# Optimization experiments

Hardware: AMD Instinct MI355X
Metric: run time of the kernel (lower is better)

Reference implementation:

```python
import jax, jax.numpy as jnp
import numpy as np
import math

B, L, D = 2, 2048, 768
H, DK = 8, 64
DV = D // H  # 96
N_POS = 32
DFF = 2 * D
EPS = 1e-5


def setup_inputs() -> dict:
    key = jax.random.key(0)
    ks = jax.random.split(key, 12)
    s = 0.02
    return {
        "x": jax.random.normal(ks[0], (B, L, D), jnp.float32),
        "norm1_w": jnp.ones((D,), jnp.float32),
        "norm2_w": jnp.ones((D,), jnp.float32),
        "wq": jax.random.normal(ks[1], (D, H * DK), jnp.float32) * s,
        "wk": jax.random.normal(ks[2], (D, H * DK), jnp.float32) * s,
        "wv": jax.random.normal(ks[3], (D, H * DV), jnp.float32) * s,
        "wo": jax.random.normal(ks[4], (H * DV, D), jnp.float32) * s,
        "bo": jnp.zeros((D,), jnp.float32),
        "u_param": jax.random.normal(ks[5], (H, DK), jnp.float32) * s,
        "v_param": jax.random.normal(ks[6], (H, DK), jnp.float32) * s,
        "w_pos": jax.random.normal(ks[7], (H, DK, N_POS), jnp.float32) * s,
        "w1": jax.random.normal(ks[8], (D, DFF), jnp.float32) * s,
        "b1": jnp.zeros((DFF,), jnp.float32),
        "w2": jax.random.normal(ks[9], (DFF, D), jnp.float32) * s,
        "b2": jnp.zeros((D,), jnp.float32),
    }


def _rel_basis(l: int, n: int) -> jnp.ndarray:
    # Enformer-style central-mask relative position basis: [l, l, n]
    pos = jnp.arange(l)
    distance = pos[None, :] - pos[:, None]  # [l, l]
    pow_rate = jnp.exp(jnp.log(jnp.float32((l + 1) / 2.0)) / (n // 2))
    center_widths = pow_rate ** jnp.arange(1, n // 2 + 1, dtype=jnp.float32)
    d = distance[:, :, None].astype(jnp.float32)
    unsigned = (jnp.abs(d) <= center_widths).astype(jnp.float32)
    signed = jnp.sign(d) * unsigned
    return jnp.concatenate([unsigned, signed], axis=-1)  # [l, l, n]


def _rmsnorm(x, w):
    norm = jnp.mean(x * x, axis=-1, keepdims=True)
    return x * jax.lax.rsqrt(norm + EPS) * w


def reference(x, norm1_w, norm2_w, wq, wk, wv, wo, bo,
              u_param, v_param, w_pos, w1, b1, w2, b2):
    b, l, _ = x.shape
    skip = x
    h1 = _rmsnorm(x, norm1_w)

    q = (h1 @ wq).reshape(b, l, H, DK)
    k = (h1 @ wk).reshape(b, l, H, DK)
    v = (h1 @ wv).reshape(b, l, H, DV)

    basis = _rel_basis(l, N_POS)  # [l, l, n]
    scale = 1.0 / math.sqrt(DK)

    # qr_term: contract q with w_pos first, then with basis (avoids [h,l,l,d] r)
    qw = jnp.einsum('bihd,hdn->bihn', q, w_pos)          # [b,l,h,n]
    qr = jnp.einsum('bihn,ijn->bhij', qw, basis)          # [b,h,l,l]
    uk = jnp.einsum('hd,bjhd->bhj', u_param, k)[:, :, None, :]  # [b,h,1,l]
    vw = jnp.einsum('hd,hdn->hn', v_param, w_pos)         # [h,n]
    vr = jnp.einsum('hn,ijn->hij', vw, basis)[None]       # [1,h,l,l]

    bias = (qr + uk + vr) * scale
    scores = jnp.einsum('bihd,bjhd->bhij', q, k) * scale + bias
    attn = jax.nn.softmax(scores, axis=-1)
    out = jnp.einsum('bhij,bjhd->bihd', attn, v)          # [b,l,h,dv]

    out = out.reshape(b, l, H * DV) @ wo + bo
    x = out + skip

    skip = x
    h2 = _rmsnorm(x, norm2_w)
    h2 = jax.nn.gelu(h2 @ w1 + b1, approximate=False) @ w2 + b2
    return h2 + skip
```

## Files before the change

### kernel.cpp

```cpp
#include <hip/hip_runtime.h>

#define B_ 2
#define L_ 2048
#define D_ 768
#define H_ 8
#define DK_ 64
#define DV_ 96
#define NPOS_ 32

typedef __attribute__((ext_vector_type(8))) __bf16 bf16x8;
typedef __attribute__((ext_vector_type(4))) __bf16 bf16x4;
typedef __attribute__((ext_vector_type(4))) float f32x4;

static __device__ __forceinline__ float bs2f(short s) {
    return (float)__builtin_bit_cast(__bf16, s);
}
static __device__ __forceinline__ short f2bs(float f) {
    return __builtin_bit_cast(short, (__bf16)f);
}

typedef __attribute__((address_space(1))) void gas_void;
typedef __attribute__((address_space(3))) void las_void;
static __device__ __forceinline__ void gload16(const short* g, char* l) {
    __builtin_amdgcn_global_load_lds((const gas_void*)g, (las_void*)l, 16, 0, 0);
}

__global__ __launch_bounds__(256) void prep_kernel(
    const float* __restrict__ wq, const float* __restrict__ wk,
    const float* __restrict__ wv, const float* __restrict__ wo,
    const float* __restrict__ w1, const float* __restrict__ w2,
    const float* __restrict__ vparam, const float* __restrict__ uparam,
    const float* __restrict__ wpos,
    short* __restrict__ wqkvT, short* __restrict__ woT,
    short* __restrict__ w1T, short* __restrict__ w2T,
    unsigned char* __restrict__ sidx, float* __restrict__ VU, float* __restrict__ VS,
    const float* __restrict__ x, const float* __restrict__ n1w, short* __restrict__ h1)
{
    __shared__ short T[64][66];
    __shared__ float vw[H_ * NPOS_];
    __shared__ float uw[H_ * NPOS_];
    __shared__ float red[4];
    int blk = blockIdx.x, tid = threadIdx.x;
    if (blk < 1056) {
        const float* W; short* Wt; int K, N, bx, by;
        if (blk < 96)       { W = wq; Wt = wqkvT;              K = 768;  N = 512;  int b = blk;       bx = b % 8;  by = b / 8; }
        else if (blk < 192) { W = wk; Wt = wqkvT + 512 * 768;  K = 768;  N = 512;  int b = blk - 96;  bx = b % 8;  by = b / 8; }
        else if (blk < 336) { W = wv; Wt = wqkvT + 1024 * 768; K = 768;  N = 768;  int b = blk - 192; bx = b % 12; by = b / 12; }
        else if (blk < 480) { W = wo; Wt = woT;                K = 768;  N = 768;  int b = blk - 336; bx = b % 12; by = b / 12; }
        else if (blk < 768) { W = w1; Wt = w1T;                K = 768;  N = 1536; int b = blk - 480; bx = b % 24; by = b / 24; }
        else                { W = w2; Wt = w2T;                K = 1536; N = 768;  int b = blk - 768; bx = b % 12; by = b / 12; }
        int n0 = bx << 6, k0 = by << 6;
        for (int idx = tid; idx < 4096; idx += 256) {
            int r = idx >> 6, c = idx & 63;
            T[c][r] = f2bs(W[(size_t)(k0 + r) * N + n0 + c]);
        }
        __syncthreads();
        for (int idx = tid; idx < 4096; idx += 256) {
            int r = idx >> 6, c = idx & 63;
            Wt[(size_t)(n0 + r) * K + k0 + c] = T[r][c];
        }
    } else if (blk == 1056) {
        float pr = expf(logf((L_ + 1) / 2.0f) / (NPOS_ / 2));
        if (tid < 16) vw[tid] = powf(pr, (float)(tid + 1));
        __syncthreads();
        for (int idx = tid; idx < 4095; idx += 256) {
            int d = idx - 2047;
            int ad = d < 0 ? -d : d;
            int c = 0;
#pragma unroll
            for (int m = 0; m < 16; ++m)
                if (vw[m] < (float)ad) c++;
            sidx[idx] = (unsigned char)(d > 0 ? c : (d < 0 ? 17 + c : 34));
        }
        __syncthreads();
        {
            int h = tid >> 5, n = tid & 31;
            float av = 0.f, au = 0.f;
            for (int d = 0; d < DK_; ++d) {
                float wp = wpos[(h * DK_ + d) * NPOS_ + n];
                av += vparam[h * DK_ + d] * wp;
                au += uparam[h * DK_ + d] * wp;
            }
            vw[tid] = av;
            uw[tid] = au;
        }
        __syncthreads();
        if (tid < H_ * 17) {
            int h = tid / 17, m = tid % 17;
            float su = 0.f, ss = 0.f;
            for (int t2 = m; t2 < 16; ++t2) {
                su += vw[h * NPOS_ + t2] - uw[h * NPOS_ + t2];
                ss += vw[h * NPOS_ + 16 + t2] - uw[h * NPOS_ + 16 + t2];
            }
            VU[h * 17 + m] = su * 0.125f;
            VS[h * 17 + m] = ss * 0.125f;
        }
    } else {
        int row = blk - 1057;
        const float* xr = x + (size_t)row * D_;
        float ss = 0.f;
        for (int c = tid; c < D_; c += 256) { float f = xr[c]; ss += f * f; }
        for (int msk = 1; msk < 64; msk <<= 1) ss += __shfl_xor(ss, msk);
        if ((tid & 63) == 0) red[tid >> 6] = ss;
        __syncthreads();
        float tot = red[0] + red[1] + red[2] + red[3];
        float sc = rsqrtf(tot * (1.f / D_) + 1e-5f);
        for (int c = tid; c < D_; c += 256)
            h1[(size_t)row * D_ + c] = f2bs(xr[c] * sc * n1w[c]);
    }
}

__global__ __launch_bounds__(256) void rmsnorm_kernel(
    const float* __restrict__ x, const float* __restrict__ wgt, short* __restrict__ out)
{
    int row = blockIdx.x, tid = threadIdx.x;
    __shared__ float red[4];
    const float* xr = x + (size_t)row * D_;
    float ss = 0.f;
    for (int c = tid; c < D_; c += 256) { float f = xr[c]; ss += f * f; }
    for (int msk = 1; msk < 64; msk <<= 1) ss += __shfl_xor(ss, msk);
    if ((tid & 63) == 0) red[tid >> 6] = ss;
    __syncthreads();
    float tot = red[0] + red[1] + red[2] + red[3];
    float sc = rsqrtf(tot * (1.f / D_) + 1e-5f);
    for (int c = tid; c < D_; c += 256)
        out[(size_t)row * D_ + c] = f2bs(xr[c] * sc * wgt[c]);
}

template<int BN>
__global__ __launch_bounds__(512, 4) void gemmx(
    const short* __restrict__ A, const short* __restrict__ Bt,
    const float* __restrict__ bias, const float* __restrict__ uadd,
    const float* __restrict__ resid, void* __restrict__ outp,
    int M, int N, int K, int act, int out_f32)
{
    constexpr int STRIDE = 16384 + BN * 128;
    __shared__ __align__(16) char ldsb[2 * STRIDE];
    int tid = threadIdx.x;
    int w = tid >> 6, lane = tid & 63, quad = lane >> 4, t = lane & 15;
    int wm = (w >> 1) << 5;
    int wn = (w & 1) * (BN / 2);
    int m0b = blockIdx.y << 7, n0b = blockIdx.x * BN;

    int srow = tid >> 3;
    int scol = ((tid & 7) ^ (srow & 7)) << 3;
    const short* aSrc0 = A + (size_t)(m0b + srow) * K + scol;
    const short* aSrc1 = A + (size_t)(m0b + 64 + srow) * K + scol;
    const short* bSrc0 = Bt + (size_t)(n0b + srow) * K + scol;
    const short* bSrc1 = Bt + (size_t)(n0b + 64 + srow) * K + scol;
    int wo1024 = w << 10;

    f32x4 acc[2][BN / 32] = {};

    gload16(aSrc0, ldsb + wo1024);
    gload16(aSrc1, ldsb + 8192 + wo1024);
    gload16(bSrc0, ldsb + 16384 + wo1024);
    if (BN == 128) gload16(bSrc1, ldsb + 16384 + 8192 + wo1024);

    int swz = (t & 7) << 4;
    int cur = 0;
    for (int kb = 0; kb < K; kb += 64) {
        __syncthreads();
        if (kb + 64 < K) {
            char* nb = ldsb + (cur ^ 1) * STRIDE;
            gload16(aSrc0 + kb + 64, nb + wo1024);
            gload16(aSrc1 + kb + 64, nb + 8192 + wo1024);
            gload16(bSrc0 + kb + 64, nb + 16384 + wo1024);
            if (BN == 128) gload16(bSrc1 + kb + 64, nb + 16384 + 8192 + wo1024);
        }
        char* Ab = ldsb + cur * STRIDE;
        char* Bb = Ab + 16384;
#pragma unroll
        for (int ks = 0; ks < 2; ++ks) {
            int cb = ((ks << 6) + (quad << 4)) ^ swz;
            bf16x8 af[2], bf[BN / 32];
#pragma unroll
            for (int ms = 0; ms < 2; ++ms)
                af[ms] = *(const bf16x8*)(Ab + (wm + ms * 16 + t) * 128 + cb);
#pragma unroll
            for (int ns = 0; ns < BN / 32; ++ns)
                bf[ns] = *(const bf16x8*)(Bb + (wn + ns * 16 + t) * 128 + cb);
#pragma unroll
            for (int ms = 0; ms < 2; ++ms)
#pragma unroll
                for (int ns = 0; ns < BN / 32; ++ns)
                    acc[ms][ns] = __builtin_amdgcn_mfma_f32_16x16x32_bf16(af[ms], bf[ns], acc[ms][ns], 0, 0, 0);
        }
        cur ^= 1;
    }
#pragma unroll
    for (int ms = 0; ms < 2; ++ms)
#pragma unroll
        for (int ns = 0; ns < BN / 32; ++ns)
#pragma unroll
            for (int r = 0; r < 4; ++r) {
                int row = m0b + wm + ms * 16 + (quad << 2) + r;
                int col = n0b + wn + ns * 16 + t;
                float v2 = acc[ms][ns][r];
                if (uadd && col < 512) v2 = 0.125f * (v2 + uadd[col]);
                if (bias) v2 += bias[col];
                if (act == 1) v2 = 0.5f * v2 * (1.f + erff(v2 * 0.70710678118654752f));
                if (resid) v2 += resid[(size_t)row * N + col];
                if (out_f32) ((float*)outp)[(size_t)row * N + col] = v2;
                else ((short*)outp)[(size_t)row * N + col] = f2bs(v2);
            }
}

__global__ __launch_bounds__(256) void qv_kernel(
    const short* __restrict__ qkv, const float* __restrict__ wpos,
    const float* __restrict__ VU, const float* __restrict__ VS,
    float* __restrict__ Tg, short* __restrict__ vT, short* __restrict__ kT)
{
    __shared__ __align__(16) char arena[69696];
    int blk = blockIdx.x, tid = threadIdx.x;
    if (blk < 512) {
        float* qw = (float*)arena;
        float* sU = (float*)(arena + 1024);
        float* sS = (float*)(arena + 1568);
        int h = tid >> 5, n = tid & 31;
        float wlr[64];
#pragma unroll
        for (int d = 0; d < DK_; ++d)
            wlr[d] = wpos[(h * DK_ + d) * NPOS_ + n];
        int r0 = blk << 3;
        for (int rr = 0; rr < 8; ++rr) {
            int row = r0 + rr;
            const short* base = qkv + (size_t)row * 1792 + h * DK_;
            float acc = 0.f;
#pragma unroll
            for (int c8 = 0; c8 < 8; ++c8) {
                bf16x8 q8 = *(const bf16x8*)(base + (c8 << 3));
#pragma unroll
                for (int e = 0; e < 8; ++e)
                    acc += (float)q8[e] * wlr[(c8 << 3) + e];
            }
            qw[tid] = acc;
            __syncthreads();
            if (tid < 136) {
                int hh = tid / 17, m = tid % 17;
                float su = 0.f, ss = 0.f;
                for (int t2 = m; t2 < 16; ++t2) { su += qw[hh * NPOS_ + t2]; ss += qw[hh * NPOS_ + 16 + t2]; }
                sU[tid] = su + VU[tid];
                sS[tid] = ss + VS[tid];
            }
            __syncthreads();
            if (tid < 280) {
                int h2 = tid / 35, s = tid % 35;
                int m = s < 17 ? s : (s < 34 ? s - 17 : 0);
                float su = sU[h2 * 17 + m], ss = sS[h2 * 17 + m];
                Tg[(size_t)row * 280 + tid] = s < 17 ? su + ss : (s < 34 ? su - ss : su);
            }
        }
    } else if (blk < 768) {
        short* T = (short*)arena;
        int vb = blk - 512;
        int bh = vb >> 4, b = bh >> 3, h = bh & 7;
        int j0 = (vb & 15) << 7;
#pragma unroll
        for (int it = 0; it < 6; ++it) {
            int idx = tid + (it << 8);
            int row = idx / 12, c8 = (idx % 12) << 3;
            *(bf16x8*)&T[row * 104 + c8] =
                *(const bf16x8*)&qkv[(size_t)(b * L_ + j0 + row) * 1792 + 1024 + h * DV_ + c8];
        }
        __syncthreads();
#pragma unroll
        for (int it = 0; it < 6; ++it) {
            int idx = tid + (it << 8);
            int sub = idx / 768;
            int rem = idx - sub * 768;
            int f = rem >> 6, l = rem & 63;
            int dv = f >> 1, ks = f & 1;
            int q = l >> 4, t = l & 15;
            bf16x8 o;
#pragma unroll
            for (int e = 0; e < 8; ++e) {
                int jl = ((e & 3) << 4) + (ks << 3) + (q << 1) + (e >> 2);
                o[e] = __builtin_bit_cast(__bf16, T[(sub * 64 + jl) * 104 + dv * 16 + t]);
            }
            int jt = ((vb & 15) << 1) + sub;
            *(bf16x8*)&vT[((((size_t)bh * 32 + jt) * 12 + f) * 64 + l) * 8] = o;
        }
    } else {
        short* T = (short*)arena;
        int vb = blk - 768;
        int bh = vb >> 4, b = bh >> 3, h = bh & 7;
        int c128 = vb & 15;
        int j0 = c128 << 7;
#pragma unroll
        for (int it = 0; it < 4; ++it) {
            int idx = tid + (it << 8);
            int row = idx >> 3, c8 = (idx & 7) << 3;
            *(bf16x8*)&T[row * 72 + c8] =
                *(const bf16x8*)&qkv[(size_t)(b * L_ + j0 + row) * 1792 + 512 + h * DK_ + c8];
        }
        __syncthreads();
#pragma unroll
        for (int it = 0; it < 4; ++it) {
            int idx = tid + (it << 8);
            int sub = idx >> 9;
            int rem = idx & 511;
            int f = rem >> 6, l = rem & 63;
            int q = l >> 4, tt = l & 15;
            bf16x8 o = *(bf16x8*)&T[(sub * 64 + (f >> 1) * 16 + tt) * 72 + ((f & 1) << 5) + (q << 3)];
            int jt = (c128 << 1) + sub;
            *(bf16x8*)&kT[((((size_t)bh * 32 + jt) * 8 + f) * 64 + l) * 8] = o;
        }
    }
}

__global__ __launch_bounds__(256, 4) void flash_kernel(
    const short* __restrict__ qkv, const short* __restrict__ kT,
    const short* __restrict__ vT, const float* __restrict__ Tg,
    const unsigned char* __restrict__ sidx_g, short* __restrict__ ao)
{
    __shared__ __align__(16) char arena[15616];
    int tid = threadIdx.x;
    int w = tid >> 6, lane = tid & 63, quad = lane >> 4, t = lane & 15;
    short* Pl = (short*)(arena + w * 2304);
    float* Tt = (float*)(arena + 9216);
    unsigned char* sidxl = (unsigned char*)(arena + 11520);

    int id = blockIdx.x;
    int bh8 = id & 7, rest = id >> 3;
    int x = rest & 127, hi = rest >> 7;
    int bh = bh8 + (hi << 3);
    int b = bh >> 3, h = bh & 7;
    int i0 = x << 4;

    for (int idx = tid; idx < 16 * 35; idx += 256) {
        int il = idx / 35, s = idx - il * 35;
        Tt[il * 36 + s] = Tg[(size_t)(b * L_ + i0 + il) * 280 + h * 35 + s];
    }
    for (int idx = tid; idx < 4095; idx += 256) sidxl[idx] = sidx_g[idx];
    __syncthreads();

    int iq = i0 + t;
    const short* qbase = qkv + (size_t)(b * L_ + iq) * 1792 + h * DK_;
    bf16x8 qf0 = *(const bf16x8*)(qbase + (quad << 3));
    bf16x8 qf1 = *(const bf16x8*)(qbase + 32 + (quad << 3));

    f32x4 O[6] = {};
    float lsum[4] = {0.f, 0.f, 0.f, 0.f};
    const short* kfb = kT + (size_t)bh * 32 * 8 * 512 + lane * 8;
    const short* vfb = vT + (size_t)bh * 32 * 12 * 512 + lane * 8;

    for (int tix = 0; tix < 8; ++tix) {
        int jt = (tix << 2) + w;
        int j0 = jt << 6;
        bf16x8 kf[8];
#pragma unroll
        for (int f = 0; f < 8; ++f)
            kf[f] = *(const bf16x8*)(kfb + ((size_t)jt * 8 + f) * 512);

        float bias[4][4];
#pragma unroll
        for (int r = 0; r < 4; ++r) {
            int il = (quad << 2) + r;
            int i = i0 + il;
            const float* Trow = &Tt[il * 36];
#pragma unroll
            for (int ct = 0; ct < 4; ++ct) {
                int j = j0 + ct * 16 + t;
                bias[r][ct] = Trow[sidxl[j - i + 2047]];
            }
        }
        __builtin_amdgcn_sched_barrier(0);

        f32x4 S[4];
        __builtin_amdgcn_s_setprio(1);
#pragma unroll
        for (int ct = 0; ct < 4; ++ct) {
            f32x4 z = {};
            z = __builtin_amdgcn_mfma_f32_16x16x32_bf16(qf0, kf[ct * 2], z, 0, 0, 0);
            S[ct] = __builtin_amdgcn_mfma_f32_16x16x32_bf16(qf1, kf[ct * 2 + 1], z, 0, 0, 0);
        }
        __builtin_amdgcn_s_setprio(0);

        bf16x8 vf[12];
#pragma unroll
        for (int f = 0; f < 12; ++f)
            vf[f] = *(const bf16x8*)(vfb + ((size_t)jt * 12 + f) * 512);
        __builtin_amdgcn_sched_barrier(0);

#pragma unroll
        for (int r = 0; r < 4; ++r) {
            int il = (quad << 2) + r;
            bf16x4 pv;
#pragma unroll
            for (int ct = 0; ct < 4; ++ct) {
                float p = __expf(S[ct][r] + bias[r][ct]);
                __bf16 pb = (__bf16)p;
                pv[ct] = pb;
                lsum[r] += (float)pb;
            }
            *(bf16x4*)&Pl[il * 72 + t * 4] = pv;
        }
        __builtin_amdgcn_s_setprio(1);
#pragma unroll
        for (int ks = 0; ks < 2; ++ks) {
            bf16x8 pa = *(bf16x8*)&Pl[t * 72 + (ks << 5) + (quad << 3)];
#pragma unroll
            for (int dv = 0; dv < 6; ++dv)
                O[dv] = __builtin_amdgcn_mfma_f32_16x16x32_bf16(pa, vf[dv * 2 + ks], O[dv], 0, 0, 0);
        }
        __builtin_amdgcn_s_setprio(0);
    }

    __syncthreads();
    float* F = (float*)arena;
    if (w >= 2) {
        int col = ((w - 2) << 6) + lane;
#pragma unroll
        for (int dv = 0; dv < 6; ++dv)
#pragma unroll
            for (int r = 0; r < 4; ++r)
                F[((dv << 2) + r) * 128 + col] = O[dv][r];
#pragma unroll
        for (int r = 0; r < 4; ++r) F[(24 + r) * 128 + col] = lsum[r];
    }
    __syncthreads();
    if (w < 2) {
        int col = (w << 6) + lane;
#pragma unroll
        for (int dv = 0; dv < 6; ++dv)
#pragma unroll
            for (int r = 0; r < 4; ++r)
                O[dv][r] += F[((dv << 2) + r) * 128 + col];
#pragma unroll
        for (int r = 0; r < 4; ++r) lsum[r] += F[(24 + r) * 128 + col];
    }
    __syncthreads();
    if (w == 1) {
        int col = 64 + lane;
#pragma unroll
        for (int dv = 0; dv < 6; ++dv)
#pragma unroll
            for (int r = 0; r < 4; ++r)
                F[((dv << 2) + r) * 128 + col] = O[dv][r];
#pragma unroll
        for (int r = 0; r < 4; ++r) F[(24 + r) * 128 + col] = lsum[r];
    }
    __syncthreads();
    if (w == 0) {
        int col = 64 + lane;
#pragma unroll
        for (int r = 0; r < 4; ++r) {
            float lr = lsum[r] + F[(24 + r) * 128 + col];
            lr += __shfl_xor(lr, 1);
            lr += __shfl_xor(lr, 2);
            lr += __shfl_xor(lr, 4);
            lr += __shfl_xor(lr, 8);
            float inv = 1.f / lr;
            int i = i0 + (quad << 2) + r;
            size_t base = (size_t)(b * L_ + i) * D_ + h * DV_;
#pragma unroll
            for (int dv = 0; dv < 6; ++dv)
                ao[base + dv * 16 + t] = f2bs((O[dv][r] + F[((dv << 2) + r) * 128 + col]) * inv);
        }
    }
}

extern "C" void kernel_launch(void* const* d_in, const int* in_sizes, int n_in,
                              void* d_out, int out_size, void* d_ws, size_t ws_size,
                              hipStream_t stream)
{
    const float* x    = (const float*)d_in[0];
    const float* n1w  = (const float*)d_in[1];
    const float* n2w  = (const float*)d_in[2];
    const float* wq   = (const float*)d_in[3];
    const float* wk   = (const float*)d_in[4];
    const float* wv   = (const float*)d_in[5];
    const float* wo   = (const float*)d_in[6];
    const float* bo   = (const float*)d_in[7];
    const float* up   = (const float*)d_in[8];
    const float* vp   = (const float*)d_in[9];
    const float* wpos = (const float*)d_in[10];
    const float* w1   = (const float*)d_in[11];
    const float* b1   = (const float*)d_in[12];
    const float* w2   = (const float*)d_in[13];
    const float* b2   = (const float*)d_in[14];

    char* ws = (char*)d_ws;
    short* h1   = (short*)(ws + 0);
    short* qkv  = (short*)(ws + 6291456);
    float* Tg   = (float*)(ws + 20971520);
    float* VUg  = (float*)(ws + 25559040);
    float* VSg  = (float*)(ws + 25560064);
    unsigned char* sidx = (unsigned char*)(ws + 25561088);
    short* ao   = (short*)(ws + 25569280);
    float* x2   = (float*)(ws + 31860736);
    short* vT   = (short*)(ws + 31860736);
    short* kT   = (short*)(ws + 38152192);
    short* wqkvT= (short*)(ws + 44443648);
    short* woT  = (short*)(ws + 47196160);
    short* w1T  = (short*)(ws + 48375808);
    short* w2T  = (short*)(ws + 50735104);
    short* f1   = (short*)(ws + 0);
    short* h2n  = (short*)(ws + 14680064);

    prep_kernel<<<5153, 256, 0, stream>>>(wq, wk, wv, wo, w1, w2, vp, up, wpos,
                                          wqkvT, woT, w1T, w2T, sidx, VUg, VSg,
                                          x, n1w, h1);
    gemmx<128><<<dim3(14, 32), 512, 0, stream>>>(h1, wqkvT, nullptr, up, nullptr, qkv, 4096, 1792, 768, 0, 0);
    qv_kernel<<<1024, 256, 0, stream>>>(qkv, wpos, VUg, VSg, Tg, vT, kT);
    flash_kernel<<<dim3(2048), 256, 0, stream>>>(qkv, kT, vT, Tg, sidx, ao);
    gemmx<64><<<dim3(12, 32), 512, 0, stream>>>(ao, woT, bo, nullptr, x, x2, 4096, 768, 768, 0, 1);
    rmsnorm_kernel<<<4096, 256, 0, stream>>>(x2, n2w, h2n);
    gemmx<128><<<dim3(12, 32), 512, 0, stream>>>(h2n, w1T, b1, nullptr, nullptr, f1, 4096, 1536, 768, 1, 0);
    gemmx<64><<<dim3(12, 32), 512, 0, stream>>>(f1, w2T, b2, nullptr, x2, d_out, 4096, 768, 1536, 0, 1);
}
```

Baseline: 286.5 us.

## Process two 16-row query tiles per flash block to reuse K/V fragments

Each flash attention block now handles 32 query rows (two 16-row groups) instead of 16, so each K and V fragment loaded from global memory feeds twice as many MFMAs, and the grid is halved. The first group's softmax/bias work is interleaved between the two S MFMA batches, giving some overlap. The cost is more registers (two O accumulators, two Q fragment sets), a lower occupancy target (launch bounds 3), a larger LDS arena, and a cross-wave reduction epilogue that now runs twice.

```diff
diff --git a/kernel.cpp b/kernel.cpp
--- a/kernel.cpp
+++ b/kernel.cpp
@@ -309,39 +309,43 @@
     }
 }
 
-__global__ __launch_bounds__(256, 4) void flash_kernel(
+__global__ __launch_bounds__(256, 3) void flash_kernel(
     const short* __restrict__ qkv, const short* __restrict__ kT,
     const short* __restrict__ vT, const float* __restrict__ Tg,
     const unsigned char* __restrict__ sidx_g, short* __restrict__ ao)
 {
-    __shared__ __align__(16) char arena[15616];
+    __shared__ __align__(16) char arena[27136];
     int tid = threadIdx.x;
     int w = tid >> 6, lane = tid & 63, quad = lane >> 4, t = lane & 15;
-    short* Pl = (short*)(arena + w * 2304);
-    float* Tt = (float*)(arena + 9216);
-    unsigned char* sidxl = (unsigned char*)(arena + 11520);
+    short* Pla = (short*)(arena + w * 4608);
+    short* Plb = (short*)(arena + w * 4608 + 2304);
+    float* Tt = (float*)(arena + 18432);
+    unsigned char* sidxl = (unsigned char*)(arena + 23040);
 
     int id = blockIdx.x;
     int bh8 = id & 7, rest = id >> 3;
-    int x = rest & 127, hi = rest >> 7;
+    int x = rest & 63, hi = rest >> 6;
     int bh = bh8 + (hi << 3);
     int b = bh >> 3, h = bh & 7;
-    int i0 = x << 4;
-
-    for (int idx = tid; idx < 16 * 35; idx += 256) {
+    int i0 = x << 5;
+
+    for (int idx = tid; idx < 32 * 35; idx += 256) {
         int il = idx / 35, s = idx - il * 35;
         Tt[il * 36 + s] = Tg[(size_t)(b * L_ + i0 + il) * 280 + h * 35 + s];
     }
     for (int idx = tid; idx < 4095; idx += 256) sidxl[idx] = sidx_g[idx];
     __syncthreads();
 
-    int iq = i0 + t;
-    const short* qbase = qkv + (size_t)(b * L_ + iq) * 1792 + h * DK_;
-    bf16x8 qf0 = *(const bf16x8*)(qbase + (quad << 3));
-    bf16x8 qf1 = *(const bf16x8*)(qbase + 32 + (quad << 3));
-
-    f32x4 O[6] = {};
-    float lsum[4] = {0.f, 0.f, 0.f, 0.f};
+    const short* qa = qkv + (size_t)(b * L_ + i0 + t) * 1792 + h * DK_;
+    const short* qb = qkv + (size_t)(b * L_ + i0 + 16 + t) * 1792 + h * DK_;
+    bf16x8 qf0a = *(const bf16x8*)(qa + (quad << 3));
+    bf16x8 qf1a = *(const bf16x8*)(qa + 32 + (quad << 3));
+    bf16x8 qf0b = *(const bf16x8*)(qb + (quad << 3));
+    bf16x8 qf1b = *(const bf16x8*)(qb + 32 + (quad << 3));
+
+    f32x4 Oa[6] = {}, Ob[6] = {};
+    float lsa[4] = {0.f, 0.f, 0.f, 0.f};
+    float lsb[4] = {0.f, 0.f, 0.f, 0.f};
     const short* kfb = kT + (size_t)bh * 32 * 8 * 512 + lane * 8;
     const short* vfb = vT + (size_t)bh * 32 * 12 * 512 + lane * 8;
 
@@ -352,28 +356,40 @@
 #pragma unroll
         for (int f = 0; f < 8; ++f)
             kf[f] = *(const bf16x8*)(kfb + ((size_t)jt * 8 + f) * 512);
-
-        float bias[4][4];
+        __builtin_amdgcn_sched_barrier(0);
+
+        f32x4 S[4];
+        __builtin_amdgcn_s_setprio(1);
+#pragma unroll
+        for (int ct = 0; ct < 4; ++ct) {
+            f32x4 z = {};
+            z = __builtin_amdgcn_mfma_f32_16x16x32_bf16(qf0a, kf[ct * 2], z, 0, 0, 0);
+            S[ct] = __builtin_amdgcn_mfma_f32_16x16x32_bf16(qf1a, kf[ct * 2 + 1], z, 0, 0, 0);
+        }
+        __builtin_amdgcn_s_setprio(0);
 #pragma unroll
         for (int r = 0; r < 4; ++r) {
             int il = (quad << 2) + r;
             int i = i0 + il;
             const float* Trow = &Tt[il * 36];
+            bf16x4 pv;
 #pragma unroll
             for (int ct = 0; ct < 4; ++ct) {
                 int j = j0 + ct * 16 + t;
-                bias[r][ct] = Trow[sidxl[j - i + 2047]];
-            }
-        }
-        __builtin_amdgcn_sched_barrier(0);
-
-        f32x4 S[4];
+                int s = sidxl[j - i + 2047];
+                float p = __expf(S[ct][r] + Trow[s]);
+                __bf16 pb = (__bf16)p;
+                pv[ct] = pb;
+                lsa[r] += (float)pb;
+            }
+            *(bf16x4*)&Pla[il * 72 + t * 4] = pv;
+        }
         __builtin_amdgcn_s_setprio(1);
 #pragma unroll
         for (int ct = 0; ct < 4; ++ct) {
             f32x4 z = {};
-            z = __builtin_amdgcn_mfma_f32_16x16x32_bf16(qf0, kf[ct * 2], z, 0, 0, 0);
-            S[ct] = __builtin_amdgcn_mfma_f32_16x16x32_bf16(qf1, kf[ct * 2 + 1], z, 0, 0, 0);
+            z = __builtin_amdgcn_mfma_f32_16x16x32_bf16(qf0b, kf[ct * 2], z, 0, 0, 0);
+            S[ct] = __builtin_amdgcn_mfma_f32_16x16x32_bf16(qf1b, kf[ct * 2 + 1], z, 0, 0, 0);
         }
         __builtin_amdgcn_s_setprio(0);
 
@@ -382,81 +398,92 @@
         for (int f = 0; f < 12; ++f)
             vf[f] = *(const bf16x8*)(vfb + ((size_t)jt * 12 + f) * 512);
         __builtin_amdgcn_sched_barrier(0);
-
 #pragma unroll
         for (int r = 0; r < 4; ++r) {
             int il = (quad << 2) + r;
+            int i = i0 + 16 + il;
+            const float* Trow = &Tt[(16 + il) * 36];
             bf16x4 pv;
 #pragma unroll
             for (int ct = 0; ct < 4; ++ct) {
-                float p = __expf(S[ct][r] + bias[r][ct]);
+                int j = j0 + ct * 16 + t;
+                int s = sidxl[j - i + 2047];
+                float p = __expf(S[ct][r] + Trow[s]);
                 __bf16 pb = (__bf16)p;
                 pv[ct] = pb;
-                lsum[r] += (float)pb;
-            }
-            *(bf16x4*)&Pl[il * 72 + t * 4] = pv;
+                lsb[r] += (float)pb;
+            }
+            *(bf16x4*)&Plb[il * 72 + t * 4] = pv;
         }
         __builtin_amdgcn_s_setprio(1);
 #pragma unroll
         for (int ks = 0; ks < 2; ++ks) {
-            bf16x8 pa = *(bf16x8*)&Pl[t * 72 + (ks << 5) + (quad << 3)];
-#pragma unroll
-            for (int dv = 0; dv < 6; ++dv)
-                O[dv] = __builtin_amdgcn_mfma_f32_16x16x32_bf16(pa, vf[dv * 2 + ks], O[dv], 0, 0, 0);
+            bf16x8 paa = *(bf16x8*)&Pla[t * 72 + (ks << 5) + (quad << 3)];
+            bf16x8 pab = *(bf16x8*)&Plb[t * 72 + (ks << 5) + (quad << 3)];
+#pragma unroll
+            for (int dv = 0; dv < 6; ++dv) {
+                Oa[dv] = __builtin_amdgcn_mfma_f32_16x16x32_bf16(paa, vf[dv * 2 + ks], Oa[dv], 0, 0, 0);
+                Ob[dv] = __builtin_amdgcn_mfma_f32_16x16x32_bf16(pab, vf[dv * 2 + ks], Ob[dv], 0, 0, 0);
+            }
         }
         __builtin_amdgcn_s_setprio(0);
     }
 
-    __syncthreads();
     float* F = (float*)arena;
-    if (w >= 2) {
-        int col = ((w - 2) << 6) + lane;
-#pragma unroll
-        for (int dv = 0; dv < 6; ++dv)
-#pragma unroll
-            for (int r = 0; r < 4; ++r)
-                F[((dv << 2) + r) * 128 + col] = O[dv][r];
-#pragma unroll
-        for (int r = 0; r < 4; ++r) F[(24 + r) * 128 + col] = lsum[r];
-    }
-    __syncthreads();
-    if (w < 2) {
-        int col = (w << 6) + lane;
-#pragma unroll
-        for (int dv = 0; dv < 6; ++dv)
-#pragma unroll
-            for (int r = 0; r < 4; ++r)
-                O[dv][r] += F[((dv << 2) + r) * 128 + col];
-#pragma unroll
-        for (int r = 0; r < 4; ++r) lsum[r] += F[(24 + r) * 128 + col];
-    }
-    __syncthreads();
-    if (w == 1) {
-        int col = 64 + lane;
-#pragma unroll
-        for (int dv = 0; dv < 6; ++dv)
-#pragma unroll
-            for (int r = 0; r < 4; ++r)
-                F[((dv << 2) + r) * 128 + col] = O[dv][r];
-#pragma unroll
-        for (int r = 0; r < 4; ++r) F[(24 + r) * 128 + col] = lsum[r];
-    }
-    __syncthreads();
-    if (w == 0) {
-        int col = 64 + lane;
-#pragma unroll
-        for (int r = 0; r < 4; ++r) {
-            float lr = lsum[r] + F[(24 + r) * 128 + col];
-            lr += __shfl_xor(lr, 1);
-            lr += __shfl_xor(lr, 2);
-            lr += __shfl_xor(lr, 4);
-            lr += __shfl_xor(lr, 8);
-            float inv = 1.f / lr;
-            int i = i0 + (quad << 2) + r;
-            size_t base = (size_t)(b * L_ + i) * D_ + h * DV_;
+#pragma unroll
+    for (int g = 0; g < 2; ++g) {
+        f32x4* O = g ? Ob : Oa;
+        float* ls = g ? lsb : lsa;
+        __syncthreads();
+        if (w >= 2) {
+            int col = ((w - 2) << 6) + lane;
 #pragma unroll
             for (int dv = 0; dv < 6; ++dv)
-                ao[base + dv * 16 + t] = f2bs((O[dv][r] + F[((dv << 2) + r) * 128 + col]) * inv);
+#pragma unroll
+                for (int r = 0; r < 4; ++r)
+                    F[((dv << 2) + r) * 128 + col] = O[dv][r];
+#pragma unroll
+            for (int r = 0; r < 4; ++r) F[(24 + r) * 128 + col] = ls[r];
+        }
+        __syncthreads();
+        if (w < 2) {
+            int col = (w << 6) + lane;
+#pragma unroll
+            for (int dv = 0; dv < 6; ++dv)
+#pragma unroll
+                for (int r = 0; r < 4; ++r)
+                    O[dv][r] += F[((dv << 2) + r) * 128 + col];
+#pragma unroll
+            for (int r = 0; r < 4; ++r) ls[r] += F[(24 + r) * 128 + col];
+        }
+        __syncthreads();
+        if (w == 1) {
+            int col = 64 + lane;
+#pragma unroll
+            for (int dv = 0; dv < 6; ++dv)
+#pragma unroll
+                for (int r = 0; r < 4; ++r)
+                    F[((dv << 2) + r) * 128 + col] = O[dv][r];
+#pragma unroll
+            for (int r = 0; r < 4; ++r) F[(24 + r) * 128 + col] = ls[r];
+        }
+        __syncthreads();
+        if (w == 0) {
+            int col = 64 + lane;
+#pragma unroll
+            for (int r = 0; r < 4; ++r) {
+                float lr = ls[r] + F[(24 + r) * 128 + col];
+                lr += __shfl_xor(lr, 1);
+                lr += __shfl_xor(lr, 2);
+                lr += __shfl_xor(lr, 4);
+                lr += __shfl_xor(lr, 8);
+                float inv = 1.f / lr;
+                int i = i0 + (g << 4) + (quad << 2) + r;
+                size_t base = (size_t)(b * L_ + i) * D_ + h * DV_;
+#pragma unroll
+                for (int dv = 0; dv < 6; ++dv)
+                    ao[base + dv * 16 + t] = f2bs((O[dv][r] + F[((dv << 2) + r) * 128 + col]) * inv);
+            }
         }
     }
 }
@@ -504,7 +531,7 @@
                                           x, n1w, h1);
     gemmx<128><<<dim3(14, 32), 512, 0, stream>>>(h1, wqkvT, nullptr, up, nullptr, qkv, 4096, 1792, 768, 0, 0);
     qv_kernel<<<1024, 256, 0, stream>>>(qkv, wpos, VUg, VSg, Tg, vT, kT);
-    flash_kernel<<<dim3(2048), 256, 0, stream>>>(qkv, kT, vT, Tg, sidx, ao);
+    flash_kernel<<<dim3(1024), 256, 0, stream>>>(qkv, kT, vT, Tg, sidx, ao);
     gemmx<64><<<dim3(12, 32), 512, 0, stream>>>(ao, woT, bo, nullptr, x, x2, 4096, 768, 768, 0, 1);
     rmsnorm_kernel<<<4096, 256, 0, stream>>>(x2, n2w, h2n);
     gemmx<128><<<dim3(12, 32), 512, 0, stream>>>(h2n, w1T, b1, nullptr, nullptr, f1, 4096, 1536, 768, 1, 0);
```

Result: faster. 273.7 us (-4.5%).
